# Performance work log

Hardware: AMD Instinct MI355X
Metric: run time of the kernel (lower is better)

The kernel has to match this reference:

```python
import jax, jax.numpy as jnp
import numpy as np

MAX_RADIUS = 3.0
NUM_BASIS = 8
NUM_NEIGHBORS = 16.0
N, E, NS, NV, B, D, T, L, HR = 2048, 32768, 32, 16, 8, 32, 32, 2, 64
NW = NS * 2 * NV + NV * 2 * (NS + NV) + NV * 2 * NV  # 3072 per-edge TP weights


def smooth_cutoff(x):
    u = 2.0 * (x - 1.0)
    y = 0.5 * (1.0 - jnp.cos(jnp.pi * u))
    y = jnp.where(u > 0, 0.0, y)
    y = jnp.where(u < -1, 1.0, y)
    return y


def bessel_basis(length):
    # soft_one_hot_linspace(basis='bessel', cutoff=False) * sqrt(NUM_BASIS)
    k = jnp.arange(1, NUM_BASIS + 1, dtype=length.dtype) * jnp.pi
    l = jnp.maximum(length, 1e-9)[..., None]
    return jnp.sqrt(2.0 / MAX_RADIUS) * jnp.sin(k * l / MAX_RADIUS) / l * np.sqrt(NUM_BASIS)


def get_edge_info(x, edge_src, edge_dst):
    n = x.shape[0]
    xr = x.reshape(n, 2, 3)                         # 2 vectors per node
    vec = xr[edge_src] - xr[edge_dst]               # [E,2,3]
    length = jnp.sqrt(jnp.sum(vec * vec, axis=-1) + 1e-12)   # [E,2]
    sh = np.sqrt(3.0) * vec / length[..., None]     # component-normalized l=1 SH
    feat = bessel_basis(length)                     # [E,2,B]
    attr = smooth_cutoff(length / MAX_RADIUS)[..., None] * sh  # [E,2,3]
    return feat.reshape(vec.shape[0], -1), attr


def setup_inputs() -> dict:
    key = jax.random.key(0)
    ks = jax.random.split(key, 20)
    inp = {
        'x': jax.random.normal(ks[0], (N, 6), jnp.float32),
        'batch': jnp.zeros((N,), jnp.int64 if jax.config.jax_enable_x64 else jnp.int32),
        'node_attr': jax.random.randint(ks[1], (N,), 0, T),
        'edge_src': jax.random.randint(ks[2], (E,), 0, N),
        'edge_dst': jax.random.randint(ks[3], (E,), 0, N),
        'emb': jax.random.normal(ks[4], (T, D), jnp.float32),
        'W_uplift': jax.random.normal(ks[5], (NV, 2), jnp.float32),
        'W_sc_s': jax.random.normal(ks[6], (L, NS, D, NS + NV), jnp.float32),
        'W_sc_v': jax.random.normal(ks[7], (L, NV, D, NV), jnp.float32),
        'W_l1_s': jax.random.normal(ks[8], (L, NS, NS), jnp.float32),
        'W_l1_v': jax.random.normal(ks[9], (L, NV, NV), jnp.float32),
        'W_r1': jax.random.normal(ks[10], (L, 2 * B, HR), jnp.float32),
        'W_r2': jax.random.normal(ks[11], (L, HR, NW), jnp.float32),
        'W_l2_s': jax.random.normal(ks[12], (L, NS + NV, NS + NV), jnp.float32),
        'W_l2_v': jax.random.normal(ks[13], (L, NV, NV), jnp.float32),
        'W_si_s': jax.random.normal(ks[14], (L, NS, NS), jnp.float32),
        'W_si_v': jax.random.normal(ks[15], (L, NV, NV), jnp.float32),
        'h': jnp.ones((L,), jnp.float32) * 0.01,
        'mix': jnp.ones((L,), jnp.float32) * 0.5,
    }
    return inp


def reference(x, batch, node_attr, edge_src, edge_dst, emb, W_uplift, W_sc_s, W_sc_v,
              W_l1_s, W_l1_v, W_r1, W_r2, W_l2_s, W_l2_v, W_si_s, W_si_v, h, mix):
    n = x.shape[0]
    a = emb[node_attr]                              # node attr embedding [N,D]
    Q, _ = jnp.linalg.qr(W_uplift)                  # semi-unitary uplift [NV,2]
    y_v = jnp.einsum('ci,nik->nck', Q, x.reshape(n, 2, 3))   # uplift vectors
    y_s = jnp.zeros((n, NS), x.dtype)
    y, y_old = (y_s, y_v), (y_s, y_v)
    n1 = NS * 2 * NV
    n2 = NV * 2 * (NS + NV)
    for i in range(L):
        ef, ea = get_edge_info(x, edge_src, edge_dst)       # [E,2B], [E,2,3]
        ys, yv = y
        # self-connection tensor product (features x node_attr)
        sc_s = jnp.einsum('ni,na,iaj->nj', ys, a, W_sc_s[i]) / np.sqrt(NS * D)
        sc_v = jnp.einsum('nck,na,caj->njk', yv, a, W_sc_v[i]) / np.sqrt(NV * D)
        # lin1
        s1 = ys @ W_l1_s[i] / np.sqrt(NS)
        v1 = jnp.einsum('nck,cj->njk', yv, W_l1_v[i]) / np.sqrt(NV)
        # radial MLP -> per-edge TP weights
        hr = jax.nn.silu(ef @ W_r1[i] / np.sqrt(2 * B))
        w = hr @ W_r2[i] / np.sqrt(HR)                       # [E,NW]
        w_sv = w[:, :n1].reshape(E, NS, 2, NV)
        w_vs = w[:, n1:n1 + n2].reshape(E, NV, 2, NS + NV)
        w_vv = w[:, n1 + n2:].reshape(E, NV, 2, NV)
        s_src, v_src = s1[edge_src], v1[edge_src]
        # edge tensor product: 0e x 1o -> 1o, 1o x 1o -> 0e (dot), 1o x 1o -> 1o (cross)
        e_v = jnp.einsum('esmj,es,emk->ejk', w_sv, s_src, ea) / np.sqrt(NS * 2)
        dots = jnp.einsum('eck,emk->ecm', v_src, ea)
        e_s = jnp.einsum('ecmj,ecm->ej', w_vs, dots) / np.sqrt(NV * 2 * 3)
        crs = jnp.cross(v_src[:, :, None, :], ea[:, None, :, :])  # [E,NV,2,3]
        e_v = e_v + jnp.einsum('ecmj,ecmk->ejk', w_vv, crs) / np.sqrt(NV * 2 * 2)
        # scatter-aggregate over destination nodes
        ns_ = jax.ops.segment_sum(e_s, edge_dst, num_segments=n) / np.sqrt(NUM_NEIGHBORS)
        nv_ = jax.ops.segment_sum(e_v, edge_dst, num_segments=n) / np.sqrt(NUM_NEIGHBORS)
        s2 = ns_ @ W_l2_s[i] / np.sqrt(NS + NV)
        v2 = jnp.einsum('nck,cj->njk', nv_, W_l2_v[i]) / np.sqrt(NV)
        conv_s, conv_v = sc_s + s2, sc_v + v2
        # gate
        g_s = jax.nn.silu(conv_s[:, :NS])
        g_v = jax.nn.sigmoid(conv_s[:, NS:])[:, :, None] * conv_v
        # self-interaction
        si_s = ys @ W_si_s[i] / np.sqrt(NS)
        si_v = jnp.einsum('nck,cj->njk', yv, W_si_v[i]) / np.sqrt(NV)
        # gated leapfrog update
        h2, m = h[i] ** 2, mix[i]
        new_s = 2 * ys - y_old[0] + h2 * (m * g_s + (m - 1) * si_s)
        new_v = 2 * yv - y_old[1] + h2 * (m * g_v + (m - 1) * si_v)
        y_old, y = y, (new_s, new_v)
        x = jnp.einsum('ci,nck->nik', Q, y[1]).reshape(n, 6)  # project back
    return x
```

## Files before the change

### kernel.cpp

```cpp
#include <hip/hip_runtime.h>
#include <hip/hip_bf16.h>
#include <math.h>

#define NN   2048
#define EE   32768
#define NS   32
#define NV   16
#define NB   8
#define DD   32
#define TT   32
#define LL   2
#define HRD  64
#define NWW  3072
#define TPE  128
#define PI_F 3.14159265358979323846f

#define SC_SCS (1.0f/32.0f)
#define SC_SCV 0.04419417382415922f
#define SC_L1S 0.17677669529663687f
#define SC_L1V 0.25f
#define SC_R1  0.25f
#define SC_R2  0.125f
#define SC_ES  0.10206207261596575f
#define SC_EV  0.125f
#define SC_AGG 0.25f
#define SC_L2S 0.14433756729740643f
#define SC_L2V 0.25f
#define SC_SIS 0.17677669529663687f
#define SC_SIV 0.25f

typedef __attribute__((ext_vector_type(8))) short  short8;
typedef __attribute__((ext_vector_type(4))) float  floatx4;

__device__ __forceinline__ void load_lds16(const void* g, void* l) {
    __builtin_amdgcn_global_load_lds(
        (const __attribute__((address_space(1))) unsigned int*)g,
        (__attribute__((address_space(3))) unsigned int*)l, 16, 0, 0);
}

__device__ __forceinline__ floatx4 mfma16(short8 a, short8 b, floatx4 c) {
    return __builtin_amdgcn_mfma_f32_16x16x32_bf16(a, b, c, 0, 0, 0);
}

__device__ __forceinline__ void seg_reduce_store(
        const float (*red)[49], const int* dst_s,
        const int* __restrict__ row_ptr, int ebase,
        int tid, int wave, int lane,
        int* segstart_s, int* wtot_s, int* nseg_s,
        float* __restrict__ outg) {
    int seg_flag = 0, seg_lidx = 0;
    if (tid < TPE) {
        seg_flag = (tid == 0) || (dst_s[tid] != dst_s[tid - 1]);
        unsigned long long m = __ballot(seg_flag != 0);
        if (lane == 0) wtot_s[wave] = (int)__popcll(m);
        seg_lidx = (int)__popcll(m & ((1ull << lane) - 1ull));
    }
    __syncthreads();
    if (seg_flag) segstart_s[seg_lidx + (wave ? wtot_s[0] : 0)] = tid;
    if (tid == 0) {
        int ns = wtot_s[0] + wtot_s[1];
        nseg_s[0] = ns;
        segstart_s[ns] = TPE;
    }
    __syncthreads();
    int nseg = nseg_s[0];
    for (int w = tid; w < nseg * 48; w += 256) {
        int seg = w / 48, c = w - seg * 48;
        int p0 = segstart_s[seg], p1 = segstart_s[seg + 1];
        int d = dst_s[p0];
        float run = 0.f;
        for (int pos = p0; pos < p1; ++pos) run += red[pos][c];
        if (row_ptr[d] >= ebase && row_ptr[d + 1] <= ebase + TPE)
            outg[d * 48 + c] = run;
        else
            atomicAdd(&outg[d * 48 + c], run);
    }
}

__global__ void k_setup(const float* __restrict__ Wup, float* __restrict__ Q,
                        const float* __restrict__ emb,
                        const float* __restrict__ Wscs, const float* __restrict__ Wscv,
                        float* __restrict__ WtS, float* __restrict__ WtV,
                        const float* __restrict__ Wr2, __hip_bfloat16* __restrict__ wr2t,
                        int* __restrict__ deg, int* __restrict__ cursor) {
    int b = blockIdx.x;
    if (b == 0) {
        if (threadIdx.x != 0) return;
        double A[16][2], tau[2];
        for (int i = 0; i < 16; ++i)
            for (int j = 0; j < 2; ++j) A[i][j] = (double)Wup[i*2 + j];
        for (int j = 0; j < 2; ++j) {
            double alpha = A[j][j];
            double xn2 = 0.0;
            for (int i = j + 1; i < 16; ++i) xn2 += A[i][j]*A[i][j];
            if (xn2 == 0.0) {
                tau[j] = 0.0;
            } else {
                double nrm  = sqrt(alpha*alpha + xn2);
                double beta = (alpha >= 0.0) ? -nrm : nrm;
                tau[j] = (beta - alpha) / beta;
                double s = 1.0 / (alpha - beta);
                for (int i = j + 1; i < 16; ++i) A[i][j] *= s;
                A[j][j] = beta;
            }
            for (int k = j + 1; k < 2; ++k) {
                double w = A[j][k];
                for (int i = j + 1; i < 16; ++i) w += A[i][j]*A[i][k];
                w *= tau[j];
                A[j][k] -= w;
                for (int i = j + 1; i < 16; ++i) A[i][k] -= A[i][j]*w;
            }
        }
        double Qm[16][2];
        for (int i = 0; i < 16; ++i)
            for (int j = 0; j < 2; ++j) Qm[i][j] = (i == j) ? 1.0 : 0.0;
        for (int j = 1; j >= 0; --j) {
            for (int k = 0; k < 2; ++k) {
                double w = Qm[j][k];
                for (int i = j + 1; i < 16; ++i) w += A[i][j]*Qm[i][k];
                w *= tau[j];
                Qm[j][k] -= w;
                for (int i = j + 1; i < 16; ++i) Qm[i][k] -= A[i][j]*w;
            }
        }
        for (int i = 0; i < 16; ++i)
            for (int j = 0; j < 2; ++j) Q[i*2 + j] = (float)Qm[i][j];
    } else if (b <= 64) {
        int lt = b - 1;
        int l = lt >> 5, t = lt & 31;
        __shared__ float es[32];
        if (threadIdx.x < 32) es[threadIdx.x] = emb[t*DD + threadIdx.x];
        __syncthreads();
        const float* Ws = Wscs + (size_t)l*NS*DD*48;
        float* oS = WtS + (size_t)(l*TT + t)*NS*48;
        for (int idx = threadIdx.x; idx < NS*48; idx += 256) {
            int i = idx / 48, j = idx % 48;
            float acc = 0.f;
            for (int a = 0; a < 32; ++a) acc += es[a]*Ws[(i*DD + a)*48 + j];
            oS[idx] = acc;
        }
        const float* Wv = Wscv + (size_t)l*NV*DD*NV;
        float* oV = WtV + (size_t)(l*TT + t)*NV*NV;
        for (int idx = threadIdx.x; idx < NV*NV; idx += 256) {
            int c = idx / 16, j = idx % 16;
            float acc = 0.f;
            for (int a = 0; a < 32; ++a) acc += es[a]*Wv[(c*DD + a)*NV + j];
            oV[idx] = acc;
        }
    } else if (b <= 1600) {
        int idx = (b - 65)*256 + threadIdx.x;
        int l = idx / (HRD*NWW);
        int r = idx - l*(HRD*NWW);
        int k = r / NWW;
        int c = r - k*NWW;
        int ch = c >> 6, cc = c & 63, q = cc >> 4, tcc = cc & 15;
        int h = k >> 5, qd = (k >> 3) & 3, j = k & 7;
        size_t dst = (size_t)l*(NWW*HRD)
                   + (size_t)((ch*32 + q*8 + h*4 + qd)*128 + tcc*8 + j);
        wr2t[dst] = __float2bfloat16(Wr2[idx]);
    } else {
        int i = (b - 1601)*256 + threadIdx.x;
        if (i < NN) { deg[i] = 0; cursor[i] = 0; }
    }
}

__global__ void k_hist(const int* __restrict__ edst, int* __restrict__ deg) {
    int e = blockIdx.x*256 + threadIdx.x;
    atomicAdd(&deg[edst[e]], 1);
}

__global__ void k_scan(const int* __restrict__ deg, int* __restrict__ row_ptr) {
    __shared__ int part[256];
    __shared__ int psc[256];
    int t = threadIdx.x;
    int loc[8]; int s = 0;
    for (int k = 0; k < 8; ++k) { loc[k] = deg[t*8 + k]; s += loc[k]; }
    part[t] = s;
    __syncthreads();
    if (t == 0) { int run = 0; for (int i = 0; i < 256; ++i) { psc[i] = run; run += part[i]; } }
    __syncthreads();
    int off = psc[t];
    for (int k = 0; k < 8; ++k) { row_ptr[t*8 + k] = off; off += loc[k]; }
    if (t == 255) row_ptr[2048] = off;
}

__global__ void k_fill(const int* __restrict__ esrc, const int* __restrict__ edst,
                       const int* __restrict__ row_ptr, int* __restrict__ cursor,
                       int* __restrict__ invperm, int* __restrict__ srcs, int* __restrict__ dsts,
                       const float* __restrict__ xin, const float* __restrict__ Q,
                       float* __restrict__ ys0, float* __restrict__ yv0,
                       float* __restrict__ ys1, float* __restrict__ yv1,
                       float* __restrict__ xcur) {
    if (blockIdx.x < 128) {
        int e = blockIdx.x*256 + threadIdx.x;
        int d = edst[e];
        int pos = atomicAdd(&cursor[d], 1);
        int p = row_ptr[d] + pos;
        invperm[e] = p;
        srcs[p] = esrc[e];
        dsts[p] = d;
    } else {
        int n = (blockIdx.x - 128)*256 + threadIdx.x;
        float xl[6];
        for (int i = 0; i < 6; ++i) { xl[i] = xin[n*6 + i]; xcur[n*6 + i] = xl[i]; }
        for (int j = 0; j < 32; ++j) { ys0[n*32 + j] = 0.f; ys1[n*32 + j] = 0.f; }
        for (int c = 0; c < 16; ++c)
            for (int k = 0; k < 3; ++k) {
                float v = Q[c*2 + 0]*xl[k] + Q[c*2 + 1]*xl[3 + k];
                yv0[n*48 + c*3 + k] = v;
                yv1[n*48 + c*3 + k] = v;
            }
    }
}

__global__ void __launch_bounds__(256) k_pre(
        const float* __restrict__ xcur,
        const int* __restrict__ esrc, const int* __restrict__ edst,
        const int* __restrict__ invperm,
        const float* __restrict__ Wr1l,
        __hip_bfloat16* __restrict__ hrg, float* __restrict__ eag,
        const float* __restrict__ ys, const float* __restrict__ yv,
        const float* __restrict__ Wl1s, const float* __restrict__ Wl1v,
        float* __restrict__ s1, float* __restrict__ v1,
        float* __restrict__ nsb, float* __restrict__ nsb2,
        float* __restrict__ nvba, float* __restrict__ nvbb) {
    if (blockIdx.x < 128) {
        __shared__ float Wr1[16*64];
        for (int i = threadIdx.x; i < 16*64; i += 256) Wr1[i] = Wr1l[i];
        __syncthreads();
        int e = blockIdx.x*256 + threadIdx.x;
        int s = esrc[e], d = edst[e];
        int p = invperm[e];
        float ef[16];
        float ea6[6];
        for (int m = 0; m < 2; ++m) {
            float v0 = xcur[s*6 + m*3 + 0] - xcur[d*6 + m*3 + 0];
            float v1_ = xcur[s*6 + m*3 + 1] - xcur[d*6 + m*3 + 1];
            float v2 = xcur[s*6 + m*3 + 2] - xcur[d*6 + m*3 + 2];
            float len = sqrtf(v0*v0 + v1_*v1_ + v2*v2 + 1e-12f);
            float inv = 1.0f/len;
            float theta = len*(PI_F/3.0f);
            float s1v = sinf(theta), c1v = cosf(theta);
            float sc  = 2.3094010767585034f*inv;
            float sp = 0.f, scur = s1v, twoc = 2.f*c1v;
            for (int bq = 0; bq < 8; ++bq) {
                ef[m*8 + bq] = sc*scur;
                float sn = twoc*scur - sp;
                sp = scur; scur = sn;
            }
            float u = 2.0f*(len*(1.0f/3.0f) - 1.0f);
            float cut;
            if (u > 0.f) cut = 0.f;
            else if (u < -1.f) cut = 1.f;
            else cut = 0.5f*(1.0f - cosf(PI_F*u));
            float shs = 1.7320508075688772f*inv*cut;
            ea6[m*3 + 0] = shs*v0;
            ea6[m*3 + 1] = shs*v1_;
            ea6[m*3 + 2] = shs*v2;
        }
        *(float2*)&eag[p*6 + 0] = make_float2(ea6[0], ea6[1]);
        *(float2*)&eag[p*6 + 2] = make_float2(ea6[2], ea6[3]);
        *(float2*)&eag[p*6 + 4] = make_float2(ea6[4], ea6[5]);
        float z[64];
        #pragma unroll
        for (int hh = 0; hh < 64; ++hh) z[hh] = 0.f;
        for (int f = 0; f < 16; ++f) {
            float efv = ef[f];
            #pragma unroll
            for (int hh = 0; hh < 64; ++hh) z[hh] += efv*Wr1[f*64 + hh];
        }
        short8* outp = (short8*)&hrg[(size_t)p*64];
        #pragma unroll
        for (int h8 = 0; h8 < 8; ++h8) {
            __hip_bfloat16 tmp[8];
            #pragma unroll
            for (int j = 0; j < 8; ++j) {
                float zz = z[h8*8 + j]*SC_R1;
                tmp[j] = __float2bfloat16(zz/(1.0f + expf(-zz)));
            }
            outp[h8] = *(short8*)tmp;
        }
    } else {
        int idx = (blockIdx.x - 128)*256 + threadIdx.x;
        int n = idx / 48, r = idx % 48;
        nsb[idx] = 0.f;
        nsb2[idx] = 0.f;
        nvba[idx] = 0.f;
        nvbb[idx] = 0.f;
        if (r < 32) {
            float acc = 0.f;
            for (int i = 0; i < 32; ++i) acc += ys[n*32 + i]*Wl1s[i*32 + r];
            s1[n*32 + r] = acc*SC_L1S;
        }
        int j = r/3, k = r - 3*j;
        float acc = 0.f;
        for (int c = 0; c < 16; ++c) acc += yv[n*48 + c*3 + k]*Wl1v[c*16 + j];
        v1[idx] = acc*SC_L1V;
    }
}

__global__ void __launch_bounds__(256, 3) k_tp(
        const __hip_bfloat16* __restrict__ hrg, const float* __restrict__ eag,
        const float* __restrict__ s1g, const float* __restrict__ v1g,
        const int* __restrict__ srcs, const int* __restrict__ dsts,
        const int* __restrict__ row_ptr,
        const __hip_bfloat16* __restrict__ wr2tl,
        float* __restrict__ nsb, float* __restrict__ nsb2,
        float* __restrict__ nvba, float* __restrict__ nvbb) {
    __shared__ __align__(16) char smem[42240];
    __shared__ float ea_s[TPE][9];
    __shared__ int   src_s[TPE];
    __shared__ int   dst_s[TPE];
    __shared__ int   segstart_s[TPE + 1];
    __shared__ int   wtot_s[2];
    __shared__ int   nseg_s[1];

    int bid = blockIdx.x;
    int region = bid % 3;
    int tile   = bid / 3;
    int ebase  = tile*TPE;
    int tid = threadIdx.x;
    int wave = tid >> 6, lane = tid & 63;
    int tc = tid & 15;
    int quad = lane >> 4;

    if (tid < TPE) { src_s[tid] = srcs[ebase + tid]; dst_s[tid] = dsts[ebase + tid]; }
    for (int i = tid; i < TPE*6; i += 256) ea_s[i/6][i%6] = eag[(size_t)ebase*6 + i];
    __syncthreads();

    const short* hr16 = (const short*)hrg;
    short8 a_lo[2], a_hi[2];
    #pragma unroll
    for (int rt = 0; rt < 2; ++rt) {
        int arow = ebase + (wave*2 + rt)*16 + tc;
        a_lo[rt] = *(const short8*)(hr16 + (size_t)arow*64 + quad*8);
        a_hi[rt] = *(const short8*)(hr16 + (size_t)arow*64 + 32 + quad*8);
    }

    const char* wb = (const char*)wr2tl;
    const float sES = SC_R2*SC_ES*SC_AGG;
    const float sEV = SC_R2*SC_EV*SC_AGG;

    char* Bbuf;
    if (region == 0)      Bbuf = smem + 16896;
    else if (region == 1) Bbuf = smem + 16896;
    else                  Bbuf = smem + 25344;

    auto stage = [&](int ch, int b) {
        const char* g = wb + (size_t)ch*8192 + wave*2048 + lane*16;
        char* l = Bbuf + b*8192 + wave*2048;
        load_lds16(g, l);
        load_lds16(g + 1024, l + 1024);
    };

    if (region == 0) {
        float (*s1t)[132] = (float(*)[132])smem;
        for (int i = tid; i < TPE*32; i += 256) {
            int e = i >> 5, s = i & 31;
            s1t[s][e] = s1g[src_s[e]*32 + s];
        }
        stage(0, 0);

        float accF[2][4][2] = {};
        for (int ci = 0; ci < 16; ++ci) {
            __syncthreads();
            if (ci + 1 < 16) stage(ci + 1, (ci + 1) & 1);
            const char* B = Bbuf + (ci & 1)*8192;
            #pragma unroll
            for (int q = 0; q < 4; ++q) {
                short8 b_lo = *(const short8*)(B + (q*8 + quad)*256 + tc*16);
                short8 b_hi = *(const short8*)(B + (q*8 + 4 + quad)*256 + tc*16);
                floatx4 c0 = {0.f,0.f,0.f,0.f}, c1 = {0.f,0.f,0.f,0.f};
                c0 = mfma16(a_lo[0], b_lo, c0); c0 = mfma16(a_hi[0], b_hi, c0);
                c1 = mfma16(a_lo[1], b_lo, c1); c1 = mfma16(a_hi[1], b_hi, c1);
                int m = q & 1;
                int sidx = ci*2 + (q >> 1);
                #pragma unroll
                for (int rt = 0; rt < 2; ++rt) {
                    int e0r = (wave*2 + rt)*16 + quad*4;
                    float4 sv = *(const float4*)&s1t[sidx][e0r];
                    floatx4 cc = rt ? c1 : c0;
                    #pragma unroll
                    for (int i = 0; i < 4; ++i)
                        accF[rt][i][m] += cc[i]*((&sv.x)[i]);
                }
            }
        }
        __syncthreads();
        float (*red)[49] = (float(*)[49])smem;
        #pragma unroll
        for (int rt = 0; rt < 2; ++rt) {
            int e0r = (wave*2 + rt)*16 + quad*4;
            #pragma unroll
            for (int i = 0; i < 4; ++i) {
                int pos = e0r + i;
                float f0 = accF[rt][i][0]*sEV, f1 = accF[rt][i][1]*sEV;
                #pragma unroll
                for (int k = 0; k < 3; ++k)
                    red[pos][tc*3 + k] = f0*ea_s[pos][k] + f1*ea_s[pos][3 + k];
            }
        }
        __syncthreads();
        seg_reduce_store((const float(*)[49])smem, dst_s, row_ptr, ebase,
                         tid, wave, lane, segstart_s, wtot_s, nseg_s, nvba);
    } else if (region == 1) {
        float (*dots_t)[132] = (float(*)[132])smem;
        float (*v1t)[132]    = (float(*)[132])(smem + 16896);
        for (int i = tid; i < TPE*48; i += 256) {
            int e = i/48, j = i%48;
            v1t[j][e] = v1g[src_s[e]*48 + j];
        }
        __syncthreads();
        for (int i = tid; i < TPE*32; i += 256) {
            int cm = i >> 7, e = i & (TPE - 1), c = cm >> 1, m = cm & 1;
            dots_t[cm][e] = v1t[c*3+0][e]*ea_s[e][m*3+0]
                          + v1t[c*3+1][e]*ea_s[e][m*3+1]
                          + v1t[c*3+2][e]*ea_s[e][m*3+2];
        }
        __syncthreads();
        stage(16, 0);

        float accES[2][4][3] = {};
        for (int ci = 16; ci < 32; ++ci) {
            __syncthreads();
            if (ci + 1 < 32) stage(ci + 1, (ci + 1) & 1);
            const char* B = Bbuf + (ci & 1)*8192;
            #pragma unroll
            for (int q = 0; q < 4; ++q) {
                short8 b_lo = *(const short8*)(B + (q*8 + quad)*256 + tc*16);
                short8 b_hi = *(const short8*)(B + (q*8 + 4 + quad)*256 + tc*16);
                floatx4 c0 = {0.f,0.f,0.f,0.f}, c1 = {0.f,0.f,0.f,0.f};
                c0 = mfma16(a_lo[0], b_lo, c0); c0 = mfma16(a_hi[0], b_hi, c0);
                c1 = mfma16(a_lo[1], b_lo, c1); c1 = mfma16(a_hi[1], b_hi, c1);
                int u = ci*4 + q - 64;
                int c = (u*10923) >> 16;
                int v6 = u - 6*c;
                int m = (v6 >= 3) ? 1 : 0;
                int g = v6 - 3*m;
                #pragma unroll
                for (int rt = 0; rt < 2; ++rt) {
                    int e0r = (wave*2 + rt)*16 + quad*4;
                    float4 dv = *(const float4*)&dots_t[c*2 + m][e0r];
                    floatx4 cc = rt ? c1 : c0;
                    #pragma unroll
                    for (int i = 0; i < 4; ++i)
                        accES[rt][i][g] += cc[i]*((&dv.x)[i]);
                }
            }
        }
        __syncthreads();
        float (*red)[49] = (float(*)[49])smem;
        #pragma unroll
        for (int rt = 0; rt < 2; ++rt) {
            int e0r = (wave*2 + rt)*16 + quad*4;
            #pragma unroll
            for (int i = 0; i < 4; ++i) {
                int pos = e0r + i;
                red[pos][tc]      = accES[rt][i][0]*sES;
                red[pos][16 + tc] = accES[rt][i][1]*sES;
                red[pos][32 + tc] = accES[rt][i][2]*sES;
            }
        }
        __syncthreads();
        seg_reduce_store((const float(*)[49])smem, dst_s, row_ptr, ebase,
                         tid, wave, lane, segstart_s, wtot_s, nseg_s, nsb);
    } else {
        float (*v1t)[132] = (float(*)[132])smem;
        for (int i = tid; i < TPE*48; i += 256) {
            int e = i/48, j = i%48;
            v1t[j][e] = v1g[src_s[e]*48 + j];
        }
        stage(32, 0);

        float accES[2][4][3] = {};
        float accV[2][4][2][3] = {};
        for (int ci = 32; ci < 48; ++ci) {
            __syncthreads();
            if (ci + 1 < 48) stage(ci + 1, (ci + 1) & 1);
            const char* B = Bbuf + (ci & 1)*8192;
            #pragma unroll
            for (int q = 0; q < 4; ++q) {
                short8 b_lo = *(const short8*)(B + (q*8 + quad)*256 + tc*16);
                short8 b_hi = *(const short8*)(B + (q*8 + 4 + quad)*256 + tc*16);
                floatx4 c0 = {0.f,0.f,0.f,0.f}, c1 = {0.f,0.f,0.f,0.f};
                c0 = mfma16(a_lo[0], b_lo, c0); c0 = mfma16(a_hi[0], b_hi, c0);
                c1 = mfma16(a_lo[1], b_lo, c1); c1 = mfma16(a_hi[1], b_hi, c1);
                if (ci < 40) {
                    int u = ci*4 + q - 64;
                    int c = (u*10923) >> 16;
                    int v6 = u - 6*c;
                    int m = (v6 >= 3) ? 1 : 0;
                    int g = v6 - 3*m;
                    #pragma unroll
                    for (int rt = 0; rt < 2; ++rt) {
                        int e0r = (wave*2 + rt)*16 + quad*4;
                        float4 vx = *(const float4*)&v1t[c*3 + 0][e0r];
                        float4 vy = *(const float4*)&v1t[c*3 + 1][e0r];
                        float4 vz = *(const float4*)&v1t[c*3 + 2][e0r];
                        floatx4 cc = rt ? c1 : c0;
                        #pragma unroll
                        for (int i = 0; i < 4; ++i) {
                            float dot = (&vx.x)[i]*ea_s[e0r + i][m*3 + 0]
                                      + (&vy.x)[i]*ea_s[e0r + i][m*3 + 1]
                                      + (&vz.x)[i]*ea_s[e0r + i][m*3 + 2];
                            accES[rt][i][g] += cc[i]*dot;
                        }
                    }
                } else {
                    int c = ci*2 - 80 + (q >> 1);
                    int m = q & 1;
                    #pragma unroll
                    for (int rt = 0; rt < 2; ++rt) {
                        int e0r = (wave*2 + rt)*16 + quad*4;
                        float4 vx = *(const float4*)&v1t[c*3 + 0][e0r];
                        float4 vy = *(const float4*)&v1t[c*3 + 1][e0r];
                        float4 vz = *(const float4*)&v1t[c*3 + 2][e0r];
                        floatx4 cc = rt ? c1 : c0;
                        #pragma unroll
                        for (int i = 0; i < 4; ++i) {
                            float ww = cc[i];
                            accV[rt][i][m][0] += ww*((&vx.x)[i]);
                            accV[rt][i][m][1] += ww*((&vy.x)[i]);
                            accV[rt][i][m][2] += ww*((&vz.x)[i]);
                        }
                    }
                }
            }
        }
        __syncthreads();
        float (*red)[49] = (float(*)[49])smem;
        #pragma unroll
        for (int rt = 0; rt < 2; ++rt) {
            int e0r = (wave*2 + rt)*16 + quad*4;
            #pragma unroll
            for (int i = 0; i < 4; ++i) {
                int pos = e0r + i;
                red[pos][tc]      = accES[rt][i][0]*sES;
                red[pos][16 + tc] = accES[rt][i][1]*sES;
                red[pos][32 + tc] = accES[rt][i][2]*sES;
            }
        }
        __syncthreads();
        seg_reduce_store((const float(*)[49])smem, dst_s, row_ptr, ebase,
                         tid, wave, lane, segstart_s, wtot_s, nseg_s, nsb2);
        __syncthreads();
        #pragma unroll
        for (int rt = 0; rt < 2; ++rt) {
            int e0r = (wave*2 + rt)*16 + quad*4;
            #pragma unroll
            for (int i = 0; i < 4; ++i) {
                int pos = e0r + i;
                float u00 = accV[rt][i][0][0], u01 = accV[rt][i][0][1], u02 = accV[rt][i][0][2];
                float u10 = accV[rt][i][1][0], u11 = accV[rt][i][1][1], u12 = accV[rt][i][1][2];
                float a0 = ea_s[pos][0], a1 = ea_s[pos][1], a2 = ea_s[pos][2];
                float b0 = ea_s[pos][3], b1 = ea_s[pos][4], b2 = ea_s[pos][5];
                red[pos][tc*3 + 0] = (u01*a2 - u02*a1 + u11*b2 - u12*b1)*sEV;
                red[pos][tc*3 + 1] = (u02*a0 - u00*a2 + u12*b0 - u10*b2)*sEV;
                red[pos][tc*3 + 2] = (u00*a1 - u01*a0 + u10*b1 - u11*b0)*sEV;
            }
        }
        __syncthreads();
        seg_reduce_store((const float(*)[49])smem, dst_s, row_ptr, ebase,
                         tid, wave, lane, segstart_s, wtot_s, nseg_s, nvbb);
    }
}

__global__ void __launch_bounds__(256) k_nodepost(
        const float* __restrict__ ysC, const float* __restrict__ yvC,
        float* __restrict__ ysO, float* __restrict__ yvO,
        const float* __restrict__ nsb, const float* __restrict__ nsb2,
        const float* __restrict__ nvba, const float* __restrict__ nvbb,
        const int* __restrict__ nattr,
        const float* __restrict__ WtSl, const float* __restrict__ WtVl,
        const float* __restrict__ Wl2s, const float* __restrict__ Wl2v,
        const float* __restrict__ Wsis, const float* __restrict__ Wsiv,
        const float* __restrict__ harr, const float* __restrict__ mixarr, int l,
        float* __restrict__ xcur, float* __restrict__ xout2,
        const float* __restrict__ Qg) {
    int wave = threadIdx.x >> 6, lane = threadIdx.x & 63;
    int n = blockIdx.x*4 + wave;
    __shared__ float ys_s[4][32], yv_s[4][48], ns_s[4][48], nv_s[4][48];
    __shared__ float cs_s[4][48], nvo_s[4][48];

    if (lane < 32) ys_s[wave][lane] = ysC[n*32 + lane];
    if (lane < 48) {
        yv_s[wave][lane] = yvC[n*48 + lane];
        ns_s[wave][lane] = nsb[n*48 + lane] + nsb2[n*48 + lane];
        nv_s[wave][lane] = nvba[n*48 + lane] + nvbb[n*48 + lane];
    }
    __syncthreads();
    int t = nattr[n];
    const float* WtSn = WtSl + (size_t)t*NS*48;
    const float* WtVn = WtVl + (size_t)t*NV*NV;
    float hv = harr[l];
    float h2 = hv*hv, mx = mixarr[l];

    if (lane < 48) {
        float sc = 0.f, s2 = 0.f;
        for (int i = 0; i < 32; ++i) sc += ys_s[wave][i]*WtSn[i*48 + lane];
        for (int c = 0; c < 48; ++c) s2 += ns_s[wave][c]*Wl2s[c*48 + lane];
        cs_s[wave][lane] = sc*SC_SCS + s2*SC_L2S;
    }
    __syncthreads();
    if (lane < 48) {
        int j = lane/3, k = lane - 3*j;
        float scv = 0.f, v2 = 0.f, siv = 0.f;
        for (int c = 0; c < 16; ++c) {
            float yvv = yv_s[wave][c*3 + k];
            scv += yvv*WtVn[c*16 + j];
            v2  += nv_s[wave][c*3 + k]*Wl2v[c*16 + j];
            siv += yvv*Wsiv[c*16 + j];
        }
        float convv = scv*SC_SCV + v2*SC_L2V;
        siv *= SC_SIV;
        float gate = 1.f/(1.f + expf(-cs_s[wave][32 + j]));
        float gv = gate*convv;
        float nvnew = 2.f*yv_s[wave][lane] - yvO[n*48 + lane] + h2*(mx*gv + (mx - 1.f)*siv);
        nvo_s[wave][lane] = nvnew;
        yvO[n*48 + lane] = nvnew;
    }
    if (lane < 32) {
        float sis = 0.f;
        for (int i = 0; i < 32; ++i) sis += ys_s[wave][i]*Wsis[i*32 + lane];
        sis *= SC_SIS;
        float cs = cs_s[wave][lane];
        float gs = cs/(1.f + expf(-cs));
        float nsnew = 2.f*ys_s[wave][lane] - ysO[n*32 + lane] + h2*(mx*gs + (mx - 1.f)*sis);
        ysO[n*32 + lane] = nsnew;
    }
    __syncthreads();
    if (lane < 6) {
        int i = lane/3, k = lane - 3*(lane/3);
        float acc = 0.f;
        for (int c = 0; c < 16; ++c) acc += Qg[c*2 + i]*nvo_s[wave][c*3 + k];
        xcur[n*6 + lane]  = acc;
        xout2[n*6 + lane] = acc;
    }
}

extern "C" void kernel_launch(void* const* d_in, const int* in_sizes, int n_in,
                              void* d_out, int out_size, void* d_ws, size_t ws_size,
                              hipStream_t stream) {
    const float* x_in  = (const float*)d_in[0];
    const int*   nattr = (const int*)  d_in[2];
    const int*   esrc  = (const int*)  d_in[3];
    const int*   edst  = (const int*)  d_in[4];
    const float* emb   = (const float*)d_in[5];
    const float* Wup   = (const float*)d_in[6];
    const float* Wscs  = (const float*)d_in[7];
    const float* Wscv  = (const float*)d_in[8];
    const float* Wl1s  = (const float*)d_in[9];
    const float* Wl1v  = (const float*)d_in[10];
    const float* Wr1   = (const float*)d_in[11];
    const float* Wr2   = (const float*)d_in[12];
    const float* Wl2s  = (const float*)d_in[13];
    const float* Wl2v  = (const float*)d_in[14];
    const float* Wsis  = (const float*)d_in[15];
    const float* Wsiv  = (const float*)d_in[16];
    const float* harr  = (const float*)d_in[17];
    const float* mixar = (const float*)d_in[18];
    float* out = (float*)d_out;

    float* ws = (float*)d_ws;
    size_t off = 0;
    float* Q    = ws + off; off += 32;
    float* WtS  = ws + off; off += (size_t)LL*TT*NS*48;
    float* WtV  = ws + off; off += (size_t)LL*TT*NV*NV;
    float* ys0  = ws + off; off += (size_t)NN*32;
    float* yv0  = ws + off; off += (size_t)NN*48;
    float* ys1  = ws + off; off += (size_t)NN*32;
    float* yv1  = ws + off; off += (size_t)NN*48;
    float* xcur = ws + off; off += (size_t)NN*6;
    float* s1   = ws + off; off += (size_t)NN*32;
    float* v1   = ws + off; off += (size_t)NN*48;
    float* nsb  = ws + off; off += (size_t)NN*48;
    float* nsb2 = ws + off; off += (size_t)NN*48;
    float* nvba = ws + off; off += (size_t)NN*48;
    float* nvbb = ws + off; off += (size_t)NN*48;
    float* eab  = ws + off; off += (size_t)EE*6;
    off = (off + 3) & ~(size_t)3;
    __hip_bfloat16* hrb  = (__hip_bfloat16*)(ws + off); off += (size_t)EE*64/2;
    __hip_bfloat16* wr2t = (__hip_bfloat16*)(ws + off); off += (size_t)LL*NWW*HRD/2;
    int* deg     = (int*)(ws + off); off += NN;
    int* cursor  = (int*)(ws + off); off += NN;
    int* row_ptr = (int*)(ws + off); off += NN + 1;
    int* invperm = (int*)(ws + off); off += EE;
    int* srcs    = (int*)(ws + off); off += EE;
    int* dsts    = (int*)(ws + off); off += EE;

    k_setup<<<1609, 256, 0, stream>>>(Wup, Q, emb, Wscs, Wscv, WtS, WtV, Wr2, wr2t,
                                      deg, cursor);
    k_hist<<<EE/256, 256, 0, stream>>>(edst, deg);
    k_scan<<<1, 256, 0, stream>>>(deg, row_ptr);
    k_fill<<<136, 256, 0, stream>>>(esrc, edst, row_ptr, cursor, invperm, srcs, dsts,
                                    x_in, Q, ys0, yv0, ys1, yv1, xcur);

    float* curS = ys0; float* curV = yv0;
    float* oldS = ys1; float* oldV = yv1;
    for (int l = 0; l < LL; ++l) {
        k_pre<<<512, 256, 0, stream>>>(xcur, esrc, edst, invperm,
                                       Wr1 + (size_t)l*16*64, hrb, eab,
                                       curS, curV, Wl1s + (size_t)l*32*32,
                                       Wl1v + (size_t)l*16*16, s1, v1,
                                       nsb, nsb2, nvba, nvbb);
        k_tp<<<3*EE/TPE, 256, 0, stream>>>(hrb, eab, s1, v1, srcs, dsts, row_ptr,
                                           wr2t + (size_t)l*NWW*HRD,
                                           nsb, nsb2, nvba, nvbb);
        float* xo2 = (l == LL - 1) ? out : xcur;
        k_nodepost<<<NN/4, 256, 0, stream>>>(curS, curV, oldS, oldV,
                                             nsb, nsb2, nvba, nvbb, nattr,
                                             WtS + (size_t)l*TT*NS*48, WtV + (size_t)l*TT*NV*NV,
                                             Wl2s + (size_t)l*48*48, Wl2v + (size_t)l*16*16,
                                             Wsis + (size_t)l*32*32, Wsiv + (size_t)l*16*16,
                                             harr, mixar, l, xcur, xo2, Q);
        float* ts = curS; curS = oldS; oldS = ts;
        float* tv = curV; curV = oldV; oldV = tv;
    }
}
```

Baseline: 252.1 us.

## Read pre-tiled radial weights directly from global and precompute dots for region 2

```diff
diff --git a/kernel.cpp b/kernel.cpp
--- a/kernel.cpp
+++ b/kernel.cpp
@@ -31,12 +31,6 @@
 
 typedef __attribute__((ext_vector_type(8))) short  short8;
 typedef __attribute__((ext_vector_type(4))) float  floatx4;
-
-__device__ __forceinline__ void load_lds16(const void* g, void* l) {
-    __builtin_amdgcn_global_load_lds(
-        (const __attribute__((address_space(1))) unsigned int*)g,
-        (__attribute__((address_space(3))) unsigned int*)l, 16, 0, 0);
-}
 
 __device__ __forceinline__ floatx4 mfma16(short8 a, short8 b, floatx4 c) {
     return __builtin_amdgcn_mfma_f32_16x16x32_bf16(a, b, c, 0, 0, 0);
@@ -341,35 +335,21 @@
     const float sES = SC_R2*SC_ES*SC_AGG;
     const float sEV = SC_R2*SC_EV*SC_AGG;
 
-    char* Bbuf;
-    if (region == 0)      Bbuf = smem + 16896;
-    else if (region == 1) Bbuf = smem + 16896;
-    else                  Bbuf = smem + 25344;
-
-    auto stage = [&](int ch, int b) {
-        const char* g = wb + (size_t)ch*8192 + wave*2048 + lane*16;
-        char* l = Bbuf + b*8192 + wave*2048;
-        load_lds16(g, l);
-        load_lds16(g + 1024, l + 1024);
-    };
-
     if (region == 0) {
         float (*s1t)[132] = (float(*)[132])smem;
         for (int i = tid; i < TPE*32; i += 256) {
             int e = i >> 5, s = i & 31;
             s1t[s][e] = s1g[src_s[e]*32 + s];
         }
-        stage(0, 0);
+        __syncthreads();
 
         float accF[2][4][2] = {};
         for (int ci = 0; ci < 16; ++ci) {
-            __syncthreads();
-            if (ci + 1 < 16) stage(ci + 1, (ci + 1) & 1);
-            const char* B = Bbuf + (ci & 1)*8192;
+            const char* Bc = wb + (size_t)ci*8192 + lane*16;
             #pragma unroll
             for (int q = 0; q < 4; ++q) {
-                short8 b_lo = *(const short8*)(B + (q*8 + quad)*256 + tc*16);
-                short8 b_hi = *(const short8*)(B + (q*8 + 4 + quad)*256 + tc*16);
+                short8 b_lo = *(const short8*)(Bc + q*2048);
+                short8 b_hi = *(const short8*)(Bc + q*2048 + 1024);
                 floatx4 c0 = {0.f,0.f,0.f,0.f}, c1 = {0.f,0.f,0.f,0.f};
                 c0 = mfma16(a_lo[0], b_lo, c0); c0 = mfma16(a_hi[0], b_hi, c0);
                 c1 = mfma16(a_lo[1], b_lo, c1); c1 = mfma16(a_hi[1], b_hi, c1);
@@ -418,17 +398,14 @@
                           + v1t[c*3+2][e]*ea_s[e][m*3+2];
         }
         __syncthreads();
-        stage(16, 0);
 
         float accES[2][4][3] = {};
         for (int ci = 16; ci < 32; ++ci) {
-            __syncthreads();
-            if (ci + 1 < 32) stage(ci + 1, (ci + 1) & 1);
-            const char* B = Bbuf + (ci & 1)*8192;
+            const char* Bc = wb + (size_t)ci*8192 + lane*16;
             #pragma unroll
             for (int q = 0; q < 4; ++q) {
-                short8 b_lo = *(const short8*)(B + (q*8 + quad)*256 + tc*16);
-                short8 b_hi = *(const short8*)(B + (q*8 + 4 + quad)*256 + tc*16);
+                short8 b_lo = *(const short8*)(Bc + q*2048);
+                short8 b_hi = *(const short8*)(Bc + q*2048 + 1024);
                 floatx4 c0 = {0.f,0.f,0.f,0.f}, c1 = {0.f,0.f,0.f,0.f};
                 c0 = mfma16(a_lo[0], b_lo, c0); c0 = mfma16(a_hi[0], b_hi, c0);
                 c1 = mfma16(a_lo[1], b_lo, c1); c1 = mfma16(a_hi[1], b_hi, c1);
@@ -465,23 +442,30 @@
         seg_reduce_store((const float(*)[49])smem, dst_s, row_ptr, ebase,
                          tid, wave, lane, segstart_s, wtot_s, nseg_s, nsb);
     } else {
-        float (*v1t)[132] = (float(*)[132])smem;
+        float (*v1t)[132]  = (float(*)[132])smem;
+        float (*dots2)[132] = (float(*)[132])(smem + 25344);
         for (int i = tid; i < TPE*48; i += 256) {
             int e = i/48, j = i%48;
             v1t[j][e] = v1g[src_s[e]*48 + j];
         }
-        stage(32, 0);
+        __syncthreads();
+        for (int i = tid; i < 12*TPE; i += 256) {
+            int r = i >> 7, e = i & (TPE - 1);
+            int c = 10 + (r >> 1), m = r & 1;
+            dots2[r][e] = v1t[c*3+0][e]*ea_s[e][m*3+0]
+                        + v1t[c*3+1][e]*ea_s[e][m*3+1]
+                        + v1t[c*3+2][e]*ea_s[e][m*3+2];
+        }
+        __syncthreads();
 
         float accES[2][4][3] = {};
         float accV[2][4][2][3] = {};
         for (int ci = 32; ci < 48; ++ci) {
-            __syncthreads();
-            if (ci + 1 < 48) stage(ci + 1, (ci + 1) & 1);
-            const char* B = Bbuf + (ci & 1)*8192;
+            const char* Bc = wb + (size_t)ci*8192 + lane*16;
             #pragma unroll
             for (int q = 0; q < 4; ++q) {
-                short8 b_lo = *(const short8*)(B + (q*8 + quad)*256 + tc*16);
-                short8 b_hi = *(const short8*)(B + (q*8 + 4 + quad)*256 + tc*16);
+                short8 b_lo = *(const short8*)(Bc + q*2048);
+                short8 b_hi = *(const short8*)(Bc + q*2048 + 1024);
                 floatx4 c0 = {0.f,0.f,0.f,0.f}, c1 = {0.f,0.f,0.f,0.f};
                 c0 = mfma16(a_lo[0], b_lo, c0); c0 = mfma16(a_hi[0], b_hi, c0);
                 c1 = mfma16(a_lo[1], b_lo, c1); c1 = mfma16(a_hi[1], b_hi, c1);
@@ -491,20 +475,15 @@
                     int v6 = u - 6*c;
                     int m = (v6 >= 3) ? 1 : 0;
                     int g = v6 - 3*m;
+                    int dr = (c - 10)*2 + m;
                     #pragma unroll
                     for (int rt = 0; rt < 2; ++rt) {
                         int e0r = (wave*2 + rt)*16 + quad*4;
-                        float4 vx = *(const float4*)&v1t[c*3 + 0][e0r];
-                        float4 vy = *(const float4*)&v1t[c*3 + 1][e0r];
-                        float4 vz = *(const float4*)&v1t[c*3 + 2][e0r];
+                        float4 dv = *(const float4*)&dots2[dr][e0r];
                         floatx4 cc = rt ? c1 : c0;
                         #pragma unroll
-                        for (int i = 0; i < 4; ++i) {
-                            float dot = (&vx.x)[i]*ea_s[e0r + i][m*3 + 0]
-                                      + (&vy.x)[i]*ea_s[e0r + i][m*3 + 1]
-                                      + (&vz.x)[i]*ea_s[e0r + i][m*3 + 2];
-                            accES[rt][i][g] += cc[i]*dot;
-                        }
+                        for (int i = 0; i < 4; ++i)
+                            accES[rt][i][g] += cc[i]*((&dv.x)[i]);
                     }
                 } else {
                     int c = ci*2 - 80 + (q >> 1);
```

Result: slower. 260.0 us (+3.1%).
